# Optimization experiments

Hardware: AMD Instinct MI355X
Metric: run time of the kernel (lower is better)

Reference implementation:

```python
import jax, jax.numpy as jnp
import numpy as np
import math

B, SQ, SK, H, NH = 8, 512, 512, 768, 12
DH = H // NH

def setup_inputs() -> dict:
    key = jax.random.key(0)
    ks = jax.random.split(key, 8)
    s = 1.0 / math.sqrt(H)
    return {
        "hidden_states": jax.random.normal(ks[0], (B, SQ, H), jnp.float32),
        "context": jax.random.normal(ks[1], (B, SK, H), jnp.float32),
        "attention_mask": jax.random.randint(ks[2], (B, SK), 0, 2, jnp.int32),
        "Wq": jax.random.normal(ks[3], (H, H), jnp.float32) * s,
        "bq": jnp.zeros((H,), jnp.float32),
        "Wk": jax.random.normal(ks[4], (H, H), jnp.float32) * s,
        "bk": jnp.zeros((H,), jnp.float32),
        "Wv": jax.random.normal(ks[5], (H, H), jnp.float32) * s,
        "bv": jnp.zeros((H,), jnp.float32),
        "abs_pos_emb": jax.random.normal(ks[6], (512, DH), jnp.float32),
    }

def _heads(x):
    # [B, S, H] -> [B, NH, S, DH]
    b, s, _ = x.shape
    return x.reshape(b, s, NH, DH).transpose(0, 2, 1, 3)

def reference(hidden_states, context, attention_mask, Wq, bq, Wk, bk, Wv, bv, abs_pos_emb):
    q = _heads(hidden_states @ Wq.T + bq)   # [B,NH,SQ,DH]
    k = _heads(context @ Wk.T + bk)         # [B,NH,SK,DH]
    v = _heads(context @ Wv.T + bv)         # [B,NH,SK,DH]
    scores = jnp.einsum('bhqd,bhkd->bhqk', q, k)
    pos_k = abs_pos_emb[:context.shape[1]]          # [SK, DH]
    pos_q = abs_pos_emb[:hidden_states.shape[1]]    # [SQ, DH]
    pos_scores = jnp.einsum('bhqd,kd->bhqk', q + pos_q[None, None], pos_k)
    scores = (scores + pos_scores) / jnp.sqrt(jnp.float32(DH))
    mask_bias = jnp.where(attention_mask[:, None, None, :] == 0,
                          -jnp.inf, 0.0).astype(scores.dtype)
    scores = scores + mask_bias
    probs = jax.nn.softmax(scores, axis=-1)  # dropout is identity in eval
    out = jnp.einsum('bhqk,bhkd->bhqd', probs, v)
    b, _, sq, _ = out.shape
    return out.transpose(0, 2, 1, 3).reshape(b, sq, NH * DH)
```

## Files before the change

kernel.cpp:

```cpp
#include <hip/hip_runtime.h>
#include <stdint.h>

#define B_   8
#define SQ_  512
#define SK_  512
#define H_   768
#define NH_  12
#define DH_  64
#define BH_  (B_*NH_)
#define M_   (B_*SQ_)
#define NTOT (3*H_)

typedef __attribute__((ext_vector_type(8))) short short8;
typedef __attribute__((ext_vector_type(4))) float floatx4;
typedef __attribute__((ext_vector_type(4))) unsigned int uint4v;
typedef __attribute__((ext_vector_type(4))) unsigned short ushort4v;

#define MFMA16(a, b, c) __builtin_amdgcn_mfma_f32_16x16x32_bf16((a), (b), (c), 0, 0, 0)

__device__ __forceinline__ unsigned short f2b(float f) {
  union { float f; unsigned u; } c; c.f = f;
  unsigned r = (c.u + 0x7fffu + ((c.u >> 16) & 1u)) >> 16;
  return (unsigned short)r;
}
__device__ __forceinline__ float b2f(unsigned short u) {
  union { float f; unsigned u; } c; c.u = ((unsigned)u) << 16;
  return c.f;
}
__device__ __forceinline__ short8 ld8(const unsigned short* p) {
  union { uint4v u; short8 s; } c;
  c.u = *(const uint4v*)p;
  return c.s;
}
__device__ __forceinline__ void gl_lds16(const unsigned short* g, unsigned short* l) {
  __builtin_amdgcn_global_load_lds(
      (const __attribute__((address_space(1))) unsigned int*)g,
      (__attribute__((address_space(3))) unsigned int*)l, 16, 0, 0);
}

#define SEG_X   (M_*H_)
#define SEG_XC  (2*SEG_X)
#define SEG_W1  (H_*H_)
#define SEG_WE  (SEG_XC + 3*SEG_W1)
#define SEG_BE  (SEG_WE + NTOT)
#define SEG_PE  (SEG_BE + SQ_*DH_)

__global__ __launch_bounds__(256) void pack_kernel(
    const float* __restrict__ hid, const float* __restrict__ ctx,
    const float* __restrict__ Wq, const float* __restrict__ Wk, const float* __restrict__ Wv,
    const float* __restrict__ bq, const float* __restrict__ bk, const float* __restrict__ bv,
    const float* __restrict__ pos,
    unsigned short* __restrict__ Xh, unsigned short* __restrict__ Xc,
    unsigned short* __restrict__ Wa, float* __restrict__ Ba,
    unsigned short* __restrict__ Pb)
{
  int i = (blockIdx.x * 256 + threadIdx.x) * 4;
  if (i < SEG_X) {
    floatx4 v = *(const floatx4*)(hid + i);
    ushort4v o = { f2b(v.x), f2b(v.y), f2b(v.z), f2b(v.w) };
    *(ushort4v*)(Xh + i) = o;
  } else if (i < SEG_XC) {
    int j = i - SEG_X;
    floatx4 v = *(const floatx4*)(ctx + j);
    ushort4v o = { f2b(v.x), f2b(v.y), f2b(v.z), f2b(v.w) };
    *(ushort4v*)(Xc + j) = o;
  } else if (i < SEG_WE) {
    int j = i - SEG_XC;
    const float* src; int o;
    if (j < SEG_W1)        { src = Wq; o = j; }
    else if (j < 2*SEG_W1) { src = Wk; o = j - SEG_W1; }
    else                   { src = Wv; o = j - 2*SEG_W1; }
    floatx4 v = *(const floatx4*)(src + o);
    ushort4v ov = { f2b(v.x), f2b(v.y), f2b(v.z), f2b(v.w) };
    *(ushort4v*)(Wa + j) = ov;
  } else if (i < SEG_BE) {
    int j = i - SEG_WE;
    #pragma unroll
    for (int t = 0; t < 4; ++t) {
      int jj = j + t;
      float v = (jj < H_) ? bq[jj] : (jj < 2*H_) ? bk[jj - H_] : bv[jj - 2*H_];
      Ba[jj] = v;
    }
  } else if (i < SEG_PE) {
    int j = i - SEG_BE;
    floatx4 v = *(const floatx4*)(pos + j);
    ushort4v o = { f2b(v.x), f2b(v.y), f2b(v.z), f2b(v.w) };
    *(ushort4v*)(Pb + j) = o;
  }
}

__global__ __launch_bounds__(256) void qkv_gemm(
    const unsigned short* __restrict__ Xh, const unsigned short* __restrict__ Xc,
    const unsigned short* __restrict__ W,  const float* __restrict__ bias,
    const unsigned short* __restrict__ Pb,
    unsigned short* __restrict__ qw, unsigned short* __restrict__ kw,
    unsigned short* __restrict__ vt)
{
  __shared__ unsigned short As[128][64];
  __shared__ unsigned short Bs[128][64];

  int bx = blockIdx.x;
  int xcd = bx & 7, j = bx >> 3;
  int bm = (xcd >> 1) * 8 + j / 9;
  int bn = (xcd & 1) * 9 + j % 9;
  const unsigned short* X = (bn < 6) ? Xh : Xc;
  bool isV = (bn >= 12);
  int m0 = bm * 128, n0 = bn * 128;

  int tid = threadIdx.x;
  int lane = tid & 63, wave = tid >> 6;
  int wm = (wave & 1) * 64, wn = (wave >> 1) * 64;
  int lc16 = lane & 15, quad = lane >> 4, kk = quad * 8;
  int srow8 = lane >> 3;
  int scol  = (lane & 7) * 8;

  unsigned short (*TA)[64] = isV ? As : Bs;
  unsigned short (*TB)[64] = isV ? Bs : As;
  int oa = isV ? wm : wn;
  int ob = isV ? wn : wm;

  floatx4 acc[4][4];
  #pragma unroll
  for (int i = 0; i < 4; ++i)
    #pragma unroll
    for (int jj = 0; jj < 4; ++jj) acc[i][jj] = (floatx4){0.f, 0.f, 0.f, 0.f};

  int rbase = wave * 32;

  for (int k0 = 0; k0 < H_; k0 += 64) {
    #pragma unroll
    for (int c = 0; c < 4; ++c) {
      int r = rbase + c * 8;
      gl_lds16(&X[(m0 + r + srow8) * H_ + k0 + scol], &As[r][0]);
      gl_lds16(&W[(n0 + r + srow8) * H_ + k0 + scol], &Bs[r][0]);
    }
    __syncthreads();

    #pragma unroll
    for (int s = 0; s < 2; ++s) {
      short8 af[4], bf[4];
      #pragma unroll
      for (int i = 0; i < 4; ++i) af[i] = ld8(&TA[oa + i * 16 + lc16][s * 32 + kk]);
      #pragma unroll
      for (int i = 0; i < 4; ++i) bf[i] = ld8(&TB[ob + i * 16 + lc16][s * 32 + kk]);
      #pragma unroll
      for (int mi = 0; mi < 4; ++mi)
        #pragma unroll
        for (int ni = 0; ni < 4; ++ni)
          acc[mi][ni] = MFMA16(af[mi], bf[ni], acc[mi][ni]);
    }
    __syncthreads();
  }

  if (!isV) {
    #pragma unroll
    for (int mi = 0; mi < 4; ++mi) {
      #pragma unroll
      for (int ni = 0; ni < 4; ++ni) {
        int gn0 = n0 + wn + mi * 16 + quad * 4;
        int gs  = m0 + wm + ni * 16 + lc16;
        int bidx = gs >> 9, s0 = gs & 511;
        floatx4 bv4 = *(const floatx4*)&bias[gn0];
        ushort4v o;
        if (gn0 < H_) {
          int h = gn0 >> 6, d0 = gn0 & 63;
          #pragma unroll
          for (int r = 0; r < 4; ++r) o[r] = f2b(acc[mi][ni][r] + bv4[r]);
          *(ushort4v*)(qw + (((bidx * NH_ + h) << 9) + s0) * DH_ + d0) = o;
        } else {
          int g = gn0 - H_;
          int h = g >> 6, d0 = g & 63;
          ushort4v pk = *(const ushort4v*)(Pb + s0 * DH_ + d0);
          #pragma unroll
          for (int r = 0; r < 4; ++r) o[r] = f2b(acc[mi][ni][r] + bv4[r] + b2f(pk[r]));
          *(ushort4v*)(kw + (((bidx * NH_ + h) << 9) + s0) * DH_ + d0) = o;
        }
      }
    }
  } else {
    #pragma unroll
    for (int mi = 0; mi < 4; ++mi) {
      #pragma unroll
      for (int ni = 0; ni < 4; ++ni) {
        int gm0 = m0 + wm + mi * 16 + quad * 4;
        int gn  = n0 + wn + ni * 16 + lc16;
        float bv = bias[gn];
        int bidx = gm0 >> 9, s0 = gm0 & 511;
        int g = gn - 2 * H_;
        int h = g >> 6, d = g & 63;
        ushort4v pk;
        #pragma unroll
        for (int r = 0; r < 4; ++r) pk[r] = f2b(acc[mi][ni][r] + bv);
        *(ushort4v*)(vt + ((bidx * NH_ + h) * DH_ + d) * SK_ + s0) = pk;
      }
    }
  }
}

#define SCALE2 0.18033688011112042f
#define CPAD 136

__global__ __launch_bounds__(256) void attn_kernel(
    const unsigned short* __restrict__ qw, const unsigned short* __restrict__ kw,
    const unsigned short* __restrict__ vt, const unsigned short* __restrict__ posb,
    const int* __restrict__ mask, float* __restrict__ out)
{
  __shared__ unsigned short Sc[2][64][CPAD];
  __shared__ float mb2[SK_];
  __shared__ float red[64][4];

  int bx = blockIdx.x;
  int bh = bx % 96, qt = bx / 96;
  int b = bh / NH_, h = bh - b * NH_;
  int tid = threadIdx.x, lane = tid & 63, wave = tid >> 6;
  int lc16 = lane & 15, quad = lane >> 4, kk = quad * 8;

  for (int i = tid; i < SK_; i += 256)
    mb2[i] = mask[(b << 9) + i] ? 0.0f : -100000.0f;

  const unsigned short* qbase = qw + ((bh << 9) + qt * 64) * DH_;
  const unsigned short* pqb   = posb + (qt * 64) * DH_;
  short8 aq[4][2], ap[4][2];
  #pragma unroll
  for (int rt = 0; rt < 4; ++rt) {
    const unsigned short* qr = qbase + (rt * 16 + lc16) * DH_;
    const unsigned short* pr = pqb + (rt * 16 + lc16) * DH_;
    aq[rt][0] = ld8(qr + kk);
    aq[rt][1] = ld8(qr + 32 + kk);
    ap[rt][0] = ld8(pr + kk);
    ap[rt][1] = ld8(pr + 32 + kk);
  }

  const unsigned short* kwb = kw + ((bh << 9)) * DH_;
  const unsigned short* vb0 = vt + (bh * DH_ + wave * 16 + lc16) * SK_;
  float rs[4] = {0.f, 0.f, 0.f, 0.f};
  floatx4 o[4];
  #pragma unroll
  for (int i = 0; i < 4; ++i) o[i] = (floatx4){0.f, 0.f, 0.f, 0.f};

  short8 cb0, cb1, cp0, cp1, nb0, nb1, np0, np1;
  {
    int kcol = wave * 32;
    const unsigned short* kb = kwb + kcol * DH_;
    const unsigned short* pb = posb + kcol * DH_;
    cb0 = ld8(kb + lc16 * DH_ + kk);
    cb1 = ld8(kb + lc16 * DH_ + 32 + kk);
    cp0 = ld8(pb + lc16 * DH_ + kk);
    cp1 = ld8(pb + lc16 * DH_ + 32 + kk);
  }

  __syncthreads();

  for (int chunk = 0; chunk < 4; ++chunk) {
    unsigned short (*S)[CPAD] = Sc[chunk & 1];

    short8 vf[4];
    #pragma unroll
    for (int ks = 0; ks < 4; ++ks) vf[ks] = ld8(vb0 + chunk * 128 + ks * 32 + kk);

    #pragma unroll
    for (int ct = 0; ct < 2; ++ct) {
      int s = chunk * 2 + ct;
      if (s < 7) {
        int kcol = ((s + 1) >> 1) * 128 + wave * 32 + ((s + 1) & 1) * 16;
        const unsigned short* kb = kwb + kcol * DH_;
        const unsigned short* pb = posb + kcol * DH_;
        nb0 = ld8(kb + lc16 * DH_ + kk);
        nb1 = ld8(kb + lc16 * DH_ + 32 + kk);
        np0 = ld8(pb + lc16 * DH_ + kk);
        np1 = ld8(pb + lc16 * DH_ + 32 + kk);
      }
      int kcol = chunk * 128 + wave * 32 + ct * 16;
      floatx4 mk = *(const floatx4*)&mb2[kcol + quad * 4];
      floatx4 c[4];
      __builtin_amdgcn_s_setprio(1);
      #pragma unroll
      for (int rt = 0; rt < 4; ++rt) {
        c[rt] = (floatx4){0.f, 0.f, 0.f, 0.f};
        c[rt] = MFMA16(cb0, aq[rt][0], c[rt]);
        c[rt] = MFMA16(cb1, aq[rt][1], c[rt]);
        c[rt] = MFMA16(cp0, ap[rt][0], c[rt]);
        c[rt] = MFMA16(cp1, ap[rt][1], c[rt]);
      }
      __builtin_amdgcn_s_setprio(0);
      int lcol = wave * 32 + ct * 16 + quad * 4;
      #pragma unroll
      for (int rt = 0; rt < 4; ++rt) {
        ushort4v pv;
        float sum = 0.f;
        #pragma unroll
        for (int r = 0; r < 4; ++r) {
          float e = __builtin_exp2f(c[rt][r] * SCALE2 + mk[r]);
          sum += e;
          pv[r] = f2b(e);
        }
        rs[rt] += sum;
        *(ushort4v*)&S[rt * 16 + lc16][lcol] = pv;
      }
      cb0 = nb0; cb1 = nb1; cp0 = np0; cp1 = np1;
    }
    __syncthreads();

    __builtin_amdgcn_s_setprio(1);
    #pragma unroll
    for (int ks = 0; ks < 4; ++ks) {
      #pragma unroll
      for (int rt = 0; rt < 4; ++rt) {
        short8 pa = ld8(&S[rt * 16 + lc16][ks * 32 + kk]);
        o[rt] = MFMA16(pa, vf[ks], o[rt]);
      }
    }
    __builtin_amdgcn_s_setprio(0);
  }

  #pragma unroll
  for (int rt = 0; rt < 4; ++rt) {
    rs[rt] += __shfl_xor(rs[rt], 16, 64);
    rs[rt] += __shfl_xor(rs[rt], 32, 64);
  }
  if (quad == 0) {
    #pragma unroll
    for (int rt = 0; rt < 4; ++rt) red[rt * 16 + lc16][wave] = rs[rt];
  }
  __syncthreads();

  #pragma unroll
  for (int rt = 0; rt < 4; ++rt) {
    #pragma unroll
    for (int r = 0; r < 4; ++r) {
      int sl = rt * 16 + quad * 4 + r;
      float inv = 1.0f / (red[sl][0] + red[sl][1] + red[sl][2] + red[sl][3]);
      int s = qt * 64 + sl;
      out[((b << 9) + s) * H_ + h * DH_ + wave * 16 + lc16] = o[rt][r] * inv;
    }
  }
}

extern "C" void kernel_launch(void* const* d_in, const int* in_sizes, int n_in,
                              void* d_out, int out_size, void* d_ws, size_t ws_size,
                              hipStream_t stream) {
  (void)in_sizes; (void)n_in; (void)out_size; (void)ws_size;
  const float* hid  = (const float*)d_in[0];
  const float* ctx  = (const float*)d_in[1];
  const int*   mask = (const int*)d_in[2];
  const float* Wq   = (const float*)d_in[3];
  const float* bq   = (const float*)d_in[4];
  const float* Wk   = (const float*)d_in[5];
  const float* bk   = (const float*)d_in[6];
  const float* Wv   = (const float*)d_in[7];
  const float* bv   = (const float*)d_in[8];
  const float* pos  = (const float*)d_in[9];

  char* ws = (char*)d_ws;
  size_t off = 0;
  auto alloc = [&](size_t bytes) { char* p = ws + off; off = (off + bytes + 255) & ~(size_t)255; return p; };
  unsigned short* Xh = (unsigned short*)alloc((size_t)SEG_X * 2);
  unsigned short* Xc = (unsigned short*)alloc((size_t)SEG_X * 2);
  unsigned short* Wa = (unsigned short*)alloc((size_t)3 * SEG_W1 * 2);
  float*          Ba = (float*)alloc((size_t)NTOT * 4);
  unsigned short* qw = (unsigned short*)alloc((size_t)BH_ * SQ_ * DH_ * 2);
  unsigned short* kw = (unsigned short*)alloc((size_t)BH_ * SK_ * DH_ * 2);
  unsigned short* vt = (unsigned short*)alloc((size_t)BH_ * DH_ * SK_ * 2);
  unsigned short* Pb = (unsigned short*)alloc((size_t)SQ_ * DH_ * 2);

  int pack_blocks = (SEG_PE / 4 + 255) / 256;
  pack_kernel<<<pack_blocks, 256, 0, stream>>>(hid, ctx, Wq, Wk, Wv, bq, bk, bv, pos, Xh, Xc, Wa, Ba, Pb);
  qkv_gemm<<<32 * 18, 256, 0, stream>>>(Xh, Xc, Wa, Ba, Pb, qw, kw, vt);
  attn_kernel<<<BH_ * 8, 256, 0, stream>>>(qw, kw, vt, Pb, mask, (float*)d_out);
}
```

Measured before the change: 166.2 us.

## Double-buffer and swizzle LDS in QKV GEMM, use packed bf16 conversions

The QKV projection GEMM now double-buffers its LDS tiles, issuing global-to-LDS loads for the next K tile before running the MFMAs on the current one. Rows are XOR-swizzled at load time so fragment reads avoid LDS bank conflicts. Float-to-bf16 conversion switches to the HIP bf16 intrinsics, including a packed two-at-a-time path in the pack kernel and epilogues. The GEMM uses twice the LDS, which may lower occupancy. The loop keeps a single barrier per iteration, so correctness relies on the end-of-iteration sync before a buffer is overwritten.

Result: faster. 159.3 us (-4.1%).

```diff
diff --git a/kernel.cpp b/kernel.cpp
--- a/kernel.cpp
+++ b/kernel.cpp
@@ -1,4 +1,5 @@
 #include <hip/hip_runtime.h>
+#include <hip/hip_bf16.h>
 #include <stdint.h>
 
 #define B_   8
@@ -19,9 +20,9 @@
 #define MFMA16(a, b, c) __builtin_amdgcn_mfma_f32_16x16x32_bf16((a), (b), (c), 0, 0, 0)
 
 __device__ __forceinline__ unsigned short f2b(float f) {
-  union { float f; unsigned u; } c; c.f = f;
-  unsigned r = (c.u + 0x7fffu + ((c.u >> 16) & 1u)) >> 16;
-  return (unsigned short)r;
+  union { __hip_bfloat16 h; unsigned short u; } c;
+  c.h = __float2bfloat16(f);
+  return c.u;
 }
 __device__ __forceinline__ float b2f(unsigned short u) {
   union { float f; unsigned u; } c; c.u = ((unsigned)u) << 16;
@@ -30,6 +31,17 @@
 __device__ __forceinline__ short8 ld8(const unsigned short* p) {
   union { uint4v u; short8 s; } c;
   c.u = *(const uint4v*)p;
+  return c.s;
+}
+__device__ __forceinline__ unsigned cvt2(float a, float b) {
+  union { __hip_bfloat162 h; unsigned u; } c;
+  c.h = __float22bfloat162_rn(float2{a, b});
+  return c.u;
+}
+__device__ __forceinline__ ushort4v cvt4(floatx4 v) {
+  union { unsigned u[2]; ushort4v s; } c;
+  c.u[0] = cvt2(v.x, v.y);
+  c.u[1] = cvt2(v.z, v.w);
   return c.s;
 }
 __device__ __forceinline__ void gl_lds16(const unsigned short* g, unsigned short* l) {
@@ -57,13 +69,11 @@
   int i = (blockIdx.x * 256 + threadIdx.x) * 4;
   if (i < SEG_X) {
     floatx4 v = *(const floatx4*)(hid + i);
-    ushort4v o = { f2b(v.x), f2b(v.y), f2b(v.z), f2b(v.w) };
-    *(ushort4v*)(Xh + i) = o;
+    *(ushort4v*)(Xh + i) = cvt4(v);
   } else if (i < SEG_XC) {
     int j = i - SEG_X;
     floatx4 v = *(const floatx4*)(ctx + j);
-    ushort4v o = { f2b(v.x), f2b(v.y), f2b(v.z), f2b(v.w) };
-    *(ushort4v*)(Xc + j) = o;
+    *(ushort4v*)(Xc + j) = cvt4(v);
   } else if (i < SEG_WE) {
     int j = i - SEG_XC;
     const float* src; int o;
@@ -71,8 +81,7 @@
     else if (j < 2*SEG_W1) { src = Wk; o = j - SEG_W1; }
     else                   { src = Wv; o = j - 2*SEG_W1; }
     floatx4 v = *(const floatx4*)(src + o);
-    ushort4v ov = { f2b(v.x), f2b(v.y), f2b(v.z), f2b(v.w) };
-    *(ushort4v*)(Wa + j) = ov;
+    *(ushort4v*)(Wa + j) = cvt4(v);
   } else if (i < SEG_BE) {
     int j = i - SEG_WE;
     #pragma unroll
@@ -84,8 +93,7 @@
   } else if (i < SEG_PE) {
     int j = i - SEG_BE;
     floatx4 v = *(const floatx4*)(pos + j);
-    ushort4v o = { f2b(v.x), f2b(v.y), f2b(v.z), f2b(v.w) };
-    *(ushort4v*)(Pb + j) = o;
+    *(ushort4v*)(Pb + j) = cvt4(v);
   }
 }
 
@@ -96,8 +104,8 @@
     unsigned short* __restrict__ qw, unsigned short* __restrict__ kw,
     unsigned short* __restrict__ vt)
 {
-  __shared__ unsigned short As[128][64];
-  __shared__ unsigned short Bs[128][64];
+  __shared__ unsigned short As[2][128][64];
+  __shared__ unsigned short Bs[2][128][64];
 
   int bx = blockIdx.x;
   int xcd = bx & 7, j = bx >> 3;
@@ -111,11 +119,11 @@
   int lane = tid & 63, wave = tid >> 6;
   int wm = (wave & 1) * 64, wn = (wave >> 1) * 64;
   int lc16 = lane & 15, quad = lane >> 4, kk = quad * 8;
-  int srow8 = lane >> 3;
-  int scol  = (lane & 7) * 8;
-
-  unsigned short (*TA)[64] = isV ? As : Bs;
-  unsigned short (*TB)[64] = isV ? Bs : As;
+
+  int srow = lane >> 3;
+  int swz  = (lane & 7) ^ srow;
+  int rb   = wave * 32;
+
   int oa = isV ? wm : wn;
   int ob = isV ? wn : wm;
 
@@ -125,24 +133,40 @@
     #pragma unroll
     for (int jj = 0; jj < 4; ++jj) acc[i][jj] = (floatx4){0.f, 0.f, 0.f, 0.f};
 
-  int rbase = wave * 32;
-
-  for (int k0 = 0; k0 < H_; k0 += 64) {
-    #pragma unroll
-    for (int c = 0; c < 4; ++c) {
-      int r = rbase + c * 8;
-      gl_lds16(&X[(m0 + r + srow8) * H_ + k0 + scol], &As[r][0]);
-      gl_lds16(&W[(n0 + r + srow8) * H_ + k0 + scol], &Bs[r][0]);
-    }
-    __syncthreads();
+  #pragma unroll
+  for (int c = 0; c < 4; ++c) {
+    int r = rb + c * 8;
+    gl_lds16(&X[(m0 + r + srow) * H_ + swz * 8], &As[0][r][0]);
+    gl_lds16(&W[(n0 + r + srow) * H_ + swz * 8], &Bs[0][r][0]);
+  }
+  __syncthreads();
+
+  for (int t = 0; t < 12; ++t) {
+    int cur = t & 1;
+    if (t < 11) {
+      int k0n = (t + 1) * 64;
+      #pragma unroll
+      for (int c = 0; c < 4; ++c) {
+        int r = rb + c * 8;
+        gl_lds16(&X[(m0 + r + srow) * H_ + k0n + swz * 8], &As[cur ^ 1][r][0]);
+        gl_lds16(&W[(n0 + r + srow) * H_ + k0n + swz * 8], &Bs[cur ^ 1][r][0]);
+      }
+    }
+
+    unsigned short (*Acur)[64] = As[cur];
+    unsigned short (*Bcur)[64] = Bs[cur];
+    unsigned short (*TA)[64] = isV ? Acur : Bcur;
+    unsigned short (*TB)[64] = isV ? Bcur : Acur;
 
     #pragma unroll
     for (int s = 0; s < 2; ++s) {
       short8 af[4], bf[4];
-      #pragma unroll
-      for (int i = 0; i < 4; ++i) af[i] = ld8(&TA[oa + i * 16 + lc16][s * 32 + kk]);
-      #pragma unroll
-      for (int i = 0; i < 4; ++i) bf[i] = ld8(&TB[ob + i * 16 + lc16][s * 32 + kk]);
+      int key = lc16 & 7;
+      int cswz = ((s * 4 + quad) ^ key) * 8;
+      #pragma unroll
+      for (int i = 0; i < 4; ++i) af[i] = ld8(&TA[oa + i * 16 + lc16][cswz]);
+      #pragma unroll
+      for (int i = 0; i < 4; ++i) bf[i] = ld8(&TB[ob + i * 16 + lc16][cswz]);
       #pragma unroll
       for (int mi = 0; mi < 4; ++mi)
         #pragma unroll
@@ -161,19 +185,20 @@
         int gs  = m0 + wm + ni * 16 + lc16;
         int bidx = gs >> 9, s0 = gs & 511;
         floatx4 bv4 = *(const floatx4*)&bias[gn0];
-        ushort4v o;
         if (gn0 < H_) {
           int h = gn0 >> 6, d0 = gn0 & 63;
+          floatx4 v;
           #pragma unroll
-          for (int r = 0; r < 4; ++r) o[r] = f2b(acc[mi][ni][r] + bv4[r]);
-          *(ushort4v*)(qw + (((bidx * NH_ + h) << 9) + s0) * DH_ + d0) = o;
+          for (int r = 0; r < 4; ++r) v[r] = acc[mi][ni][r] + bv4[r];
+          *(ushort4v*)(qw + (((bidx * NH_ + h) << 9) + s0) * DH_ + d0) = cvt4(v);
         } else {
           int g = gn0 - H_;
           int h = g >> 6, d0 = g & 63;
           ushort4v pk = *(const ushort4v*)(Pb + s0 * DH_ + d0);
+          floatx4 v;
           #pragma unroll
-          for (int r = 0; r < 4; ++r) o[r] = f2b(acc[mi][ni][r] + bv4[r] + b2f(pk[r]));
-          *(ushort4v*)(kw + (((bidx * NH_ + h) << 9) + s0) * DH_ + d0) = o;
+          for (int r = 0; r < 4; ++r) v[r] = acc[mi][ni][r] + bv4[r] + b2f(pk[r]);
+          *(ushort4v*)(kw + (((bidx * NH_ + h) << 9) + s0) * DH_ + d0) = cvt4(v);
         }
       }
     }
@@ -184,14 +209,14 @@
       for (int ni = 0; ni < 4; ++ni) {
         int gm0 = m0 + wm + mi * 16 + quad * 4;
         int gn  = n0 + wn + ni * 16 + lc16;
-        float bv = bias[gn];
+        float bvs = bias[gn];
         int bidx = gm0 >> 9, s0 = gm0 & 511;
         int g = gn - 2 * H_;
         int h = g >> 6, d = g & 63;
-        ushort4v pk;
+        floatx4 v;
         #pragma unroll
-        for (int r = 0; r < 4; ++r) pk[r] = f2b(acc[mi][ni][r] + bv);
-        *(ushort4v*)(vt + ((bidx * NH_ + h) * DH_ + d) * SK_ + s0) = pk;
+        for (int r = 0; r < 4; ++r) v[r] = acc[mi][ni][r] + bvs;
+        *(ushort4v*)(vt + ((bidx * NH_ + h) * DH_ + d) * SK_ + s0) = cvt4(v);
       }
     }
   }
```
